# Optimization experiments

Hardware: AMD Instinct MI355X
Metric: run time of the kernel (lower is better)

## Reference

```python
import jax, jax.numpy as jnp
import numpy as np

# Pangu-Weather EarthSpecificBlock, layer-1 config
WZ, WH, WW = 2, 6, 12          # window size (z, lat, lon)
Z, H, W = 8, 91, 180           # token grid after patch embedding
C = 192                        # token dim
HEADS = 6
B = 1
PAD_TOP, PAD_BOT = 2, 3        # lat 91 -> 96 (CustomPad3d, centered)
ZP, HP, WP = 8, 96, 180        # padded grid
NWB = (ZP // WZ) * (HP // WH)  # 64 bias windows (z*lat)
N = WZ * WH * WW               # 144 tokens per window


def earth_position_index():
    zi = np.arange(WZ); zj = -np.arange(WZ) * WZ
    hi = np.arange(WH); hj = -np.arange(WH) * WH
    w = np.arange(WW)
    c1 = np.stack(np.meshgrid(zi, hi, w, indexing='ij')).reshape(3, -1)
    c2 = np.stack(np.meshgrid(zj, hj, w, indexing='ij')).reshape(3, -1)
    coords = (c1[:, :, None] - c2[:, None, :]).transpose(1, 2, 0).astype(np.int64)
    coords[:, :, 2] += WW - 1
    coords[:, :, 1] *= 2 * WW - 1
    coords[:, :, 0] *= (2 * WW - 1) * WH * WH
    return coords.sum(-1)  # (N, N) int indices into bias table

POS_IDX = jnp.asarray(earth_position_index())


def layer_norm(x, w, b, eps=1e-5):
    mu = x.mean(-1, keepdims=True)
    var = ((x - mu) ** 2).mean(-1, keepdims=True)
    return (x - mu) * jax.lax.rsqrt(var + eps) * w + b


def setup_inputs() -> dict:
    key = jax.random.key(0)
    ks = jax.random.split(key, 8)
    f = lambda k, s: jax.random.normal(k, s, jnp.float32) * 0.02
    return {
        "x": jax.random.normal(ks[0], (B, Z * H * W, C), jnp.float32),
        "qkv_w": f(ks[1], (3 * C, C)),
        "qkv_b": jnp.zeros((3 * C,), jnp.float32),
        "proj_w": f(ks[2], (C, C)),
        "proj_b": jnp.zeros((C,), jnp.float32),
        "bias_table": f(ks[3], ((2 * WW - 1) * WH * WH * WZ * WZ, NWB, HEADS)),
        "norm1_w": jnp.ones((C,), jnp.float32),
        "norm1_b": jnp.zeros((C,), jnp.float32),
        "norm2_w": jnp.ones((C,), jnp.float32),
        "norm2_b": jnp.zeros((C,), jnp.float32),
        "mlp_w1": f(ks[4], (4 * C, C)),
        "mlp_b1": jnp.zeros((4 * C,), jnp.float32),
        "mlp_w2": f(ks[5], (C, 4 * C)),
        "mlp_b2": jnp.zeros((C,), jnp.float32),
        "roll": 0,
    }


def reference(x, qkv_w, qkv_b, proj_w, proj_b, bias_table,
              norm1_w, norm1_b, norm2_w, norm2_b,
              mlp_w1, mlp_b1, mlp_w2, mlp_b2, roll):
    shortcut = x  # (B, L, C)
    hd = C // HEADS
    scale = hd ** -0.5
    xs = x.reshape(B, Z, H, W, C)
    xs = jnp.pad(xs, ((0, 0), (0, 0), (PAD_TOP, PAD_BOT), (0, 0), (0, 0)))
    # window partition: (B, ZP, HP, WP, C) -> (nb, N, C), windows ordered (z, lat, lon)
    xw = xs.reshape(B, ZP // WZ, WZ, HP // WH, WH, WP // WW, WW, C)
    xw = xw.transpose(0, 1, 3, 5, 2, 4, 6, 7).reshape(-1, N, C)
    nb = xw.shape[0]  # B * 64 * 15 = 960
    qkv = (xw @ qkv_w.T + qkv_b).reshape(nb, N, 3, HEADS, hd).transpose(2, 0, 3, 1, 4)
    q, k, v = qkv[0] * scale, qkv[1], qkv[2]  # each (nb, HEADS, N, hd)
    att = jnp.einsum('bhnd,bhmd->bhnm', q, k)  # (nb, HEADS, N, N)
    # earth-specific bias gathered via position index
    bias = bias_table[POS_IDX]                 # (N, N, NWB, HEADS)
    bias = bias.transpose(2, 3, 0, 1)          # (NWB, HEADS, N, N)
    # nb = B * NWB * n_lon_windows, NWB is the leading window factor
    att = att.reshape(B, NWB, -1, HEADS, N, N) + bias[None, :, None]
    att = jax.nn.softmax(att, axis=-1).reshape(nb, HEADS, N, N)
    out = jnp.einsum('bhnm,bhmd->bnhd', att, v).reshape(nb, N, C)
    out = out @ proj_w.T + proj_b
    # window reverse + crop padding
    out = out.reshape(B, ZP // WZ, HP // WH, WP // WW, WZ, WH, WW, C)
    out = out.transpose(0, 1, 4, 2, 5, 3, 6, 7).reshape(B, ZP, HP, WP, C)
    out = out[:, :, PAD_TOP:HP - PAD_BOT, :, :].reshape(B, -1, C)
    # post-norm residual (Pangu): x = shortcut + norm1(attn); x = x + norm2(mlp(x))
    x1 = shortcut + layer_norm(out, norm1_w, norm1_b)
    h1 = jax.nn.gelu(x1 @ mlp_w1.T + mlp_b1, approximate=False)
    mlp_out = h1 @ mlp_w2.T + mlp_b2
    return x1 + layer_norm(mlp_out, norm2_w, norm2_b)
```

## Files before the change

kernel.cpp:

```cpp
#include <hip/hip_runtime.h>
#include <hip/hip_bf16.h>

typedef __hip_bfloat16 bf16;
#define DEVI __device__ __forceinline__

typedef __bf16 bf16x8 __attribute__((ext_vector_type(8)));
typedef __bf16 bf16x4 __attribute__((ext_vector_type(4)));
typedef float  f32x4  __attribute__((ext_vector_type(4)));

DEVI float bf2f(bf16 v) { return __bfloat162float(v); }
DEVI bf16 f2bf(float v) { return __float2bfloat16(v); }

DEVI unsigned short bfbits(float x) {
    bf16 h = __float2bfloat16(x);
    return *reinterpret_cast<unsigned short*>(&h);
}
DEVI unsigned int pack2(float x, float y) {
    return (unsigned int)bfbits(x) | ((unsigned int)bfbits(y) << 16);
}
DEVI float2 unpack2(unsigned int u) {
    float2 r;
    r.x = __uint_as_float(u << 16);
    r.y = __uint_as_float(u & 0xffff0000u);
    return r;
}
DEVI bf16x8 pack8(float4 lo, float4 hi) {
    union { unsigned int u[4]; bf16x8 v; } z;
    z.u[0] = pack2(lo.x, lo.y); z.u[1] = pack2(lo.z, lo.w);
    z.u[2] = pack2(hi.x, hi.y); z.u[3] = pack2(hi.z, hi.w);
    return z.v;
}
DEVI bf16x8 ld8h(const bf16* p) {
    bf16x4 lo = *(const bf16x4*)p;
    bf16x4 hi = *(const bf16x4*)(p + 4);
    return __builtin_shufflevector(lo, hi, 0, 1, 2, 3, 4, 5, 6, 7);
}

__global__ __launch_bounds__(256) void prep_attn_w(
    const float* __restrict__ qkv_w, const float* __restrict__ qkv_b,
    bf16* __restrict__ qkv_wb, float* __restrict__ qkv_bb)
{
    const float scale = 0.17677669529663687f;
    int idx = blockIdx.x * 256 + threadIdx.x;
    if (idx < 110592) {
        int c = idx % 192, d = idx / 192;
        int h = d / 96, q2 = d - h * 96, seg = q2 >> 5, rr = q2 & 31;
        float v = qkv_w[(size_t)(seg * 192 + h * 32 + rr) * 192 + c];
        if (seg == 0) v *= scale;
        qkv_wb[idx] = f2bf(v);
    }
    if (idx < 576) {
        int h = idx / 96, q2 = idx - h * 96, seg = q2 >> 5, rr = q2 & 31;
        float b = qkv_b[seg * 192 + h * 32 + rr];
        if (seg == 0) b *= scale;
        qkv_bb[idx] = b;
    }
}

__global__ __launch_bounds__(256) void prep_bias(
    const float* __restrict__ bias_table, bf16* __restrict__ biasT)
{
    int idx = blockIdx.x * 256 + threadIdx.x;
    if (idx >= 7962624) return;
    int m = idx % 144;
    int n = (idx / 144) % 144;
    int r2 = idx / 20736;
    int h = r2 % 6, wb = r2 / 6;
    int tzn = n / 72, thn = (n / 12) % 6, twn = n % 12;
    int tzm = m / 72, thm = (m / 12) % 6, twm = m % 12;
    int bidx = (tzn + 2 * tzm) * 828 + (thn + 6 * thm) * 23 + (twn - twm + 11);
    biasT[idx] = f2bf(bias_table[(size_t)(bidx * 64 + wb) * 6 + h]);
}

__global__ __launch_bounds__(256, 2) void attn_mfma_kernel(
    const float* __restrict__ x, const bf16* __restrict__ qkv_wb,
    const float* __restrict__ qkv_bb, const bf16* __restrict__ biasT,
    bf16* __restrict__ attn_out)
{
    __shared__ alignas(16) char sm[79872];
    bf16* Qs  = (bf16*)sm;
    bf16* Ks  = (bf16*)(sm + 10368);
    bf16* VTs = (bf16*)(sm + 20736);
    bf16* Ps  = (bf16*)(sm + 31488);

    const int tid  = threadIdx.x;
    const int wave = tid >> 6;
    const int lane = tid & 63;
    const int quad = lane >> 4;
    const int l15  = lane & 15;
    const int wi   = blockIdx.x;
    const int head = blockIdx.y;
    const int ww_  = wi % 15;
    const int hw   = (wi / 15) % 16;
    const int zw   = wi / 240;
    const int wb   = zw * 16 + hw;

    for (int i = tid; i < 32 * 24; i += 256) {
        int d = i / 24, c = i - d * 24;
        VTs[d * 168 + 144 + c] = f2bf(0.f);
    }

    bf16x8 af[3][6];
#pragma unroll
    for (int i = 0; i < 3; ++i) {
        int mt = wave + 4 * i;
        if (mt < 9) {
            int t  = mt * 16 + l15;
            int tz = t / 72, rr = t - tz * 72;
            int th = rr / 12, tw = rr - th * 12;
            int lat = hw * 6 + th - 2;
            bool valid = (lat >= 0 && lat < 91);
            size_t base = ((size_t)((zw * 2 + tz) * 91 + (valid ? lat : 0)) * 180
                           + ww_ * 12 + tw) * 192;
#pragma unroll
            for (int ks = 0; ks < 6; ++ks) {
                float4 lo = make_float4(0.f, 0.f, 0.f, 0.f);
                float4 hi = make_float4(0.f, 0.f, 0.f, 0.f);
                if (valid) {
                    lo = *(const float4*)(x + base + ks * 32 + quad * 8);
                    hi = *(const float4*)(x + base + ks * 32 + quad * 8 + 4);
                }
                af[i][ks] = pack8(lo, hi);
            }
        }
    }

    for (int nt = 0; nt < 6; ++nt) {
        const bf16* wrow = qkv_wb + (size_t)(head * 96 + nt * 16 + l15) * 192;
        bf16x8 bw[6];
#pragma unroll
        for (int ks = 0; ks < 6; ++ks)
            bw[ks] = *(const bf16x8*)(wrow + ks * 32 + quad * 8);
        float bias = qkv_bb[head * 96 + nt * 16 + l15];

        f32x4 acc[3];
#pragma unroll
        for (int i = 0; i < 3; ++i) acc[i] = (f32x4){0.f, 0.f, 0.f, 0.f};
#pragma unroll
        for (int ks = 0; ks < 6; ++ks)
#pragma unroll
            for (int i = 0; i < 3; ++i) {
                int mt = wave + 4 * i;
                if (mt < 9)
                    acc[i] = __builtin_amdgcn_mfma_f32_16x16x32_bf16(
                        af[i][ks], bw[ks], acc[i], 0, 0, 0);
            }
#pragma unroll
        for (int i = 0; i < 3; ++i) {
            int mt = wave + 4 * i;
            if (mt < 9) {
#pragma unroll
                for (int r = 0; r < 4; ++r) {
                    float v = acc[i][r] + bias;
                    int tok = mt * 16 + quad * 4 + r;
                    if (nt < 2)      Qs[tok * 36 + nt * 16 + l15] = f2bf(v);
                    else if (nt < 4) Ks[tok * 36 + (nt - 2) * 16 + l15] = f2bf(v);
                    else             VTs[((nt - 4) * 16 + l15) * 168 + tok] = f2bf(v);
                }
            }
        }
    }
    __syncthreads();

    bf16x8 qa[3];
#pragma unroll
    for (int i = 0; i < 3; ++i) {
        int mt = wave + 4 * i;
        if (mt < 9) qa[i] = ld8h(Qs + (mt * 16 + l15) * 36 + quad * 8);
    }
    f32x4 sa[3][9];
    for (int nt = 0; nt < 9; ++nt) {
        bf16x8 kb = ld8h(Ks + (nt * 16 + l15) * 36 + quad * 8);
#pragma unroll
        for (int i = 0; i < 3; ++i) {
            int mt = wave + 4 * i;
            sa[i][nt] = (f32x4){0.f, 0.f, 0.f, 0.f};
            if (mt < 9)
                sa[i][nt] = __builtin_amdgcn_mfma_f32_16x16x32_bf16(
                    qa[i], kb, sa[i][nt], 0, 0, 0);
        }
    }
    const bf16* bt = biasT + (size_t)(wb * 6 + head) * 20736;
#pragma unroll
    for (int i = 0; i < 3; ++i) {
        int mt = wave + 4 * i;
        if (mt < 9) {
#pragma unroll
            for (int nt = 0; nt < 9; ++nt)
#pragma unroll
                for (int r = 0; r < 4; ++r) {
                    int row = mt * 16 + quad * 4 + r;
                    sa[i][nt][r] += bf2f(bt[row * 144 + nt * 16 + l15]);
                }
        }
    }

#pragma unroll
    for (int i = 0; i < 3; ++i) {
        int mt = wave + 4 * i;
        if (mt < 9) {
#pragma unroll
            for (int r = 0; r < 4; ++r) {
                float mx = -1e30f;
#pragma unroll
                for (int nt = 0; nt < 9; ++nt) mx = fmaxf(mx, sa[i][nt][r]);
#pragma unroll
                for (int msk = 1; msk < 16; msk <<= 1)
                    mx = fmaxf(mx, __shfl_xor(mx, msk, 64));
                float s = 0.f;
#pragma unroll
                for (int nt = 0; nt < 9; ++nt) {
                    float e = __expf(sa[i][nt][r] - mx);
                    sa[i][nt][r] = e;
                    s += e;
                }
#pragma unroll
                for (int msk = 1; msk < 16; msk <<= 1)
                    s += __shfl_xor(s, msk, 64);
                float inv = 1.f / s;
                int row = mt * 16 + quad * 4 + r;
#pragma unroll
                for (int nt = 0; nt < 9; ++nt)
                    Ps[row * 168 + nt * 16 + l15] = f2bf(sa[i][nt][r] * inv);
                Ps[row * 168 + 144 + l15] = f2bf(0.f);
            }
        }
    }

    f32x4 oa[3][2];
#pragma unroll
    for (int i = 0; i < 3; ++i)
#pragma unroll
        for (int n2 = 0; n2 < 2; ++n2) oa[i][n2] = (f32x4){0.f, 0.f, 0.f, 0.f};
#pragma unroll
    for (int ks = 0; ks < 5; ++ks) {
        bf16x8 vb[2];
#pragma unroll
        for (int n2 = 0; n2 < 2; ++n2)
            vb[n2] = *(const bf16x8*)(VTs + (n2 * 16 + l15) * 168 + ks * 32 + quad * 8);
#pragma unroll
        for (int i = 0; i < 3; ++i) {
            int mt = wave + 4 * i;
            if (mt < 9) {
                bf16x8 pa = *(const bf16x8*)(Ps + (mt * 16 + l15) * 168 + ks * 32 + quad * 8);
#pragma unroll
                for (int n2 = 0; n2 < 2; ++n2)
                    oa[i][n2] = __builtin_amdgcn_mfma_f32_16x16x32_bf16(
                        pa, vb[n2], oa[i][n2], 0, 0, 0);
            }
        }
    }

#pragma unroll
    for (int i = 0; i < 3; ++i) {
        int mt = wave + 4 * i;
        if (mt < 9) {
#pragma unroll
            for (int n2 = 0; n2 < 2; ++n2)
#pragma unroll
                for (int r = 0; r < 4; ++r) {
                    int tok = mt * 16 + quad * 4 + r;
                    attn_out[(size_t)(wi * 144 + tok) * 192 + (head << 5) + n2 * 16 + l15]
                        = f2bf(oa[i][n2][r]);
                }
        }
    }
}

__global__ __launch_bounds__(256, 2) void proj_mfma_kernel(
    const bf16* __restrict__ attn, const float* __restrict__ proj_w,
    const float* __restrict__ proj_b, const float* __restrict__ xin,
    const float* __restrict__ n1w, const float* __restrict__ n1b,
    bf16* __restrict__ x1out)
{
    __shared__ alignas(16) char sm[56320];
    bf16*  Xs     = (bf16*)sm;
    float* wsum   = (float*)(sm + 51200);
    float* wsq    = (float*)(sm + 53248);
    float* mean_s = (float*)(sm + 55296);
    float* rstd_s = (float*)(sm + 55808);

    const int tid  = threadIdx.x;
    const int wave = tid >> 6;
    const int lane = tid & 63;
    const int quad = lane >> 4;
    const int l15  = lane & 15;
    const long tok0 = (long)blockIdx.x * 128;
    const int colw = wave * 48;

    for (int i = tid; i < 128 * 24; i += 256) {
        int r = i / 24, c4 = i - r * 24;
        long l = tok0 + r;
        uint4 v = make_uint4(0u, 0u, 0u, 0u);
        if (l < 131040) {
            int li  = (int)l;
            int z   = li / 16380, rem = li - z * 16380;
            int lat = rem / 180, lon = rem - lat * 180;
            int latp = lat + 2;
            int zw = z >> 1, tz = z & 1;
            int hw = latp / 6, th = latp - hw * 6;
            int wwn = lon / 12, tw = lon - wwn * 12;
            int wi = (zw * 16 + hw) * 15 + wwn;
            int t  = (tz * 6 + th) * 12 + tw;
            v = *(const uint4*)(attn + (size_t)(wi * 144 + t) * 192 + c4 * 8);
        }
        *(uint4*)(Xs + r * 200 + c4 * 8) = v;
    }
    __syncthreads();

    f32x4 o[3][8];
#pragma unroll
    for (int nt = 0; nt < 3; ++nt)
#pragma unroll
        for (int mt = 0; mt < 8; ++mt)
            o[nt][mt] = (f32x4){0.f, 0.f, 0.f, 0.f};

#pragma unroll
    for (int ks = 0; ks < 6; ++ks) {
        bf16x8 wfr[3];
#pragma unroll
        for (int nt = 0; nt < 3; ++nt) {
            const float* wp = proj_w + (size_t)(colw + nt * 16 + l15) * 192
                            + ks * 32 + quad * 8;
            float4 lo = *(const float4*)wp;
            float4 hi = *(const float4*)(wp + 4);
            wfr[nt] = pack8(lo, hi);
        }
#pragma unroll
        for (int mt = 0; mt < 8; ++mt) {
            bf16x8 a = *(const bf16x8*)(Xs + (mt * 16 + l15) * 200 + ks * 32 + quad * 8);
#pragma unroll
            for (int nt = 0; nt < 3; ++nt)
                o[nt][mt] = __builtin_amdgcn_mfma_f32_16x16x32_bf16(
                    a, wfr[nt], o[nt][mt], 0, 0, 0);
        }
    }

    float pbv[3], gw[3], gb[3];
#pragma unroll
    for (int nt = 0; nt < 3; ++nt) {
        int c = colw + nt * 16 + l15;
        pbv[nt] = proj_b[c];
        gw[nt]  = n1w[c];
        gb[nt]  = n1b[c];
    }
#pragma unroll
    for (int nt = 0; nt < 3; ++nt)
#pragma unroll
        for (int mt = 0; mt < 8; ++mt)
#pragma unroll
            for (int r = 0; r < 4; ++r)
                o[nt][mt][r] += pbv[nt];

#pragma unroll
    for (int mt = 0; mt < 8; ++mt) {
#pragma unroll
        for (int r = 0; r < 4; ++r) {
            float p = o[0][mt][r] + o[1][mt][r] + o[2][mt][r];
            float q = o[0][mt][r] * o[0][mt][r] + o[1][mt][r] * o[1][mt][r]
                    + o[2][mt][r] * o[2][mt][r];
#pragma unroll
            for (int m_ = 1; m_ < 16; m_ <<= 1) {
                p += __shfl_xor(p, m_, 64);
                q += __shfl_xor(q, m_, 64);
            }
            if (l15 == 0) {
                int row = mt * 16 + quad * 4 + r;
                wsum[row * 4 + wave] = p;
                wsq [row * 4 + wave] = q;
            }
        }
    }
    __syncthreads();
    if (tid < 128) {
        float s  = wsum[tid * 4] + wsum[tid * 4 + 1] + wsum[tid * 4 + 2] + wsum[tid * 4 + 3];
        float ss = wsq [tid * 4] + wsq [tid * 4 + 1] + wsq [tid * 4 + 2] + wsq [tid * 4 + 3];
        float m = s * (1.f / 192.f);
        float var = ss * (1.f / 192.f) - m * m;
        mean_s[tid] = m;
        rstd_s[tid] = rsqrtf(fmaxf(var, 0.f) + 1e-5f);
    }
    __syncthreads();

#pragma unroll
    for (int mt = 0; mt < 8; ++mt) {
#pragma unroll
        for (int r = 0; r < 4; ++r) {
            int row = mt * 16 + quad * 4 + r;
            long tok = tok0 + row;
            if (tok < 131040) {
                float m = mean_s[row], rsd = rstd_s[row];
#pragma unroll
                for (int nt = 0; nt < 3; ++nt) {
                    int c = colw + nt * 16 + l15;
                    float val = (o[nt][mt][r] - m) * rsd * gw[nt] + gb[nt]
                              + xin[(size_t)tok * 192 + c];
                    x1out[(size_t)tok * 192 + c] = f2bf(val);
                }
            }
        }
    }
}

__global__ __launch_bounds__(256) void prep_weights(
    const float* __restrict__ w1, const float* __restrict__ w2,
    unsigned int* __restrict__ w1b, unsigned int* __restrict__ w2b)
{
    int i = blockIdx.x * 256 + threadIdx.x;
    if (i < 73728) {
        w1b[i] = pack2(w1[2 * i], w1[2 * i + 1]);
    } else {
        int j = i - 73728;
        w2b[j] = pack2(w2[2 * j], w2[2 * j + 1]);
    }
}

__global__ __launch_bounds__(256, 2) void mlp_mfma_kernel(
    const bf16* __restrict__ x1, const bf16* __restrict__ w1b,
    const float* __restrict__ b1, const bf16* __restrict__ w2b,
    const float* __restrict__ b2, const float* __restrict__ n2w,
    const float* __restrict__ n2b, float* __restrict__ out)
{
    __shared__ alignas(16) char sm[53760];
    bf16*  Xs     = (bf16*)sm;
    bf16*  Hs     = (bf16*)(sm + 25600);
    float* wsum   = (float*)(sm + 51200);
    float* wsq    = (float*)(sm + 52224);
    float* mean_s = (float*)(sm + 53248);
    float* rstd_s = (float*)(sm + 53504);

    const int tid  = threadIdx.x;
    const int wave = tid >> 6;
    const int lane = tid & 63;
    const int quad = lane >> 4;
    const int l15  = lane & 15;
    const long tok0 = (long)blockIdx.x * 64;
    const int colw = wave * 48;

    for (int i = tid; i < 64 * 24; i += 256) {
        int r = i / 24, c8 = i - r * 24;
        uint4 v = make_uint4(0u, 0u, 0u, 0u);
        if (tok0 + r < 131040)
            v = *(const uint4*)(x1 + (tok0 + r) * 192 + (size_t)c8 * 8);
        *(uint4*)(Xs + r * 200 + c8 * 8) = v;
    }
    __syncthreads();

    bf16x8 af[4][6];
#pragma unroll
    for (int mt = 0; mt < 4; ++mt)
#pragma unroll
        for (int ks = 0; ks < 6; ++ks)
            af[mt][ks] = *(const bf16x8*)(Xs + (mt * 16 + l15) * 200 + ks * 32 + quad * 8);

    f32x4 o[3][4];
#pragma unroll
    for (int nt = 0; nt < 3; ++nt)
#pragma unroll
        for (int mt = 0; mt < 4; ++mt)
            o[nt][mt] = (f32x4){0.f, 0.f, 0.f, 0.f};

    for (int nc = 0; nc < 4; ++nc) {
        f32x4 g[3][4];
#pragma unroll
        for (int nt = 0; nt < 3; ++nt)
#pragma unroll
            for (int mt = 0; mt < 4; ++mt)
                g[nt][mt] = (f32x4){0.f, 0.f, 0.f, 0.f};
        const int h0 = nc * 192 + colw;
#pragma unroll
        for (int ks = 0; ks < 6; ++ks) {
            bf16x8 bfr[3];
#pragma unroll
            for (int nt = 0; nt < 3; ++nt)
                bfr[nt] = *(const bf16x8*)(w1b + (size_t)(h0 + nt * 16 + l15) * 192 + ks * 32 + quad * 8);
#pragma unroll
            for (int nt = 0; nt < 3; ++nt)
#pragma unroll
                for (int mt = 0; mt < 4; ++mt)
                    g[nt][mt] = __builtin_amdgcn_mfma_f32_16x16x32_bf16(
                        af[mt][ks], bfr[nt], g[nt][mt], 0, 0, 0);
        }
        __syncthreads();

#pragma unroll
        for (int nt = 0; nt < 3; ++nt) {
            float bb = b1[h0 + nt * 16 + l15];
            int hcol = colw + nt * 16 + l15;
#pragma unroll
            for (int mt = 0; mt < 4; ++mt) {
#pragma unroll
                for (int r = 0; r < 4; ++r) {
                    float v = g[nt][mt][r] + bb;
                    float u = v * (0.7978845608028654f + 0.035677408136300125f * v * v);
                    float e = __expf(2.f * u);
                    float t = 1.f - 2.f / (e + 1.f);
                    float gl = 0.5f * v * (1.f + t);
                    Hs[(mt * 16 + quad * 4 + r) * 200 + hcol] = f2bf(gl);
                }
            }
        }
        __syncthreads();

#pragma unroll
        for (int ks = 0; ks < 6; ++ks) {
            bf16x8 hf[4];
#pragma unroll
            for (int mt = 0; mt < 4; ++mt)
                hf[mt] = *(const bf16x8*)(Hs + (mt * 16 + l15) * 200 + ks * 32 + quad * 8);
            bf16x8 wf[3];
#pragma unroll
            for (int nt = 0; nt < 3; ++nt)
                wf[nt] = *(const bf16x8*)(w2b + (size_t)(colw + nt * 16 + l15) * 768 + nc * 192 + ks * 32 + quad * 8);
#pragma unroll
            for (int nt = 0; nt < 3; ++nt)
#pragma unroll
                for (int mt = 0; mt < 4; ++mt)
                    o[nt][mt] = __builtin_amdgcn_mfma_f32_16x16x32_bf16(
                        hf[mt], wf[nt], o[nt][mt], 0, 0, 0);
        }
    }

    float b2v[3], gw[3], gb[3];
#pragma unroll
    for (int nt = 0; nt < 3; ++nt) {
        int c = colw + nt * 16 + l15;
        b2v[nt] = b2[c];
        gw[nt] = n2w[c];
        gb[nt] = n2b[c];
    }
#pragma unroll
    for (int nt = 0; nt < 3; ++nt)
#pragma unroll
        for (int mt = 0; mt < 4; ++mt)
#pragma unroll
            for (int r = 0; r < 4; ++r)
                o[nt][mt][r] += b2v[nt];

#pragma unroll
    for (int mt = 0; mt < 4; ++mt) {
#pragma unroll
        for (int r = 0; r < 4; ++r) {
            float p = o[0][mt][r] + o[1][mt][r] + o[2][mt][r];
            float q = o[0][mt][r] * o[0][mt][r] + o[1][mt][r] * o[1][mt][r]
                    + o[2][mt][r] * o[2][mt][r];
#pragma unroll
            for (int m_ = 1; m_ < 16; m_ <<= 1) {
                p += __shfl_xor(p, m_, 64);
                q += __shfl_xor(q, m_, 64);
            }
            if (l15 == 0) {
                int row = mt * 16 + quad * 4 + r;
                wsum[row * 4 + wave] = p;
                wsq [row * 4 + wave] = q;
            }
        }
    }
    __syncthreads();
    if (tid < 64) {
        float s  = wsum[tid * 4] + wsum[tid * 4 + 1] + wsum[tid * 4 + 2] + wsum[tid * 4 + 3];
        float ss = wsq [tid * 4] + wsq [tid * 4 + 1] + wsq [tid * 4 + 2] + wsq [tid * 4 + 3];
        float m = s * (1.f / 192.f);
        float var = ss * (1.f / 192.f) - m * m;
        mean_s[tid] = m;
        rstd_s[tid] = rsqrtf(fmaxf(var, 0.f) + 1e-5f);
    }
    __syncthreads();

#pragma unroll
    for (int mt = 0; mt < 4; ++mt) {
#pragma unroll
        for (int r = 0; r < 4; ++r) {
            int row = mt * 16 + quad * 4 + r;
            long tok = tok0 + row;
            if (tok < 131040) {
                float m = mean_s[row], rsd = rstd_s[row];
#pragma unroll
                for (int nt = 0; nt < 3; ++nt) {
                    int c = colw + nt * 16 + l15;
                    float val = (o[nt][mt][r] - m) * rsd * gw[nt] + gb[nt]
                              + bf2f(Xs[row * 200 + c]);
                    out[tok * 192 + c] = val;
                }
            }
        }
    }
}

extern "C" void kernel_launch(void* const* d_in, const int* in_sizes, int n_in,
                              void* d_out, int out_size, void* d_ws, size_t ws_size,
                              hipStream_t stream) {
    (void)in_sizes; (void)n_in; (void)out_size; (void)ws_size;
    const float* x          = (const float*)d_in[0];
    const float* qkv_w      = (const float*)d_in[1];
    const float* qkv_b      = (const float*)d_in[2];
    const float* proj_w     = (const float*)d_in[3];
    const float* proj_b     = (const float*)d_in[4];
    const float* bias_table = (const float*)d_in[5];
    const float* n1w        = (const float*)d_in[6];
    const float* n1b        = (const float*)d_in[7];
    const float* n2w        = (const float*)d_in[8];
    const float* n2b        = (const float*)d_in[9];
    const float* w1         = (const float*)d_in[10];
    const float* b1         = (const float*)d_in[11];
    const float* w2         = (const float*)d_in[12];
    const float* b2         = (const float*)d_in[13];
    float* out = (float*)d_out;

    bf16*  attn_ws = (bf16*)d_ws;
    bf16*  x1_ws   = (bf16*)((char*)d_ws + 53084160);
    bf16*  w1b     = (bf16*)d_ws;
    bf16*  w2b     = (bf16*)((char*)d_ws + 294912);
    bf16*  qkv_wb  = (bf16*)((char*)d_ws + 53084160);
    float* qkv_bb  = (float*)((char*)d_ws + 53305344);
    bf16*  biasT   = (bf16*)((char*)d_ws + 53307648);

    prep_attn_w<<<432, 256, 0, stream>>>(qkv_w, qkv_b, qkv_wb, qkv_bb);
    prep_bias<<<31104, 256, 0, stream>>>(bias_table, biasT);
    attn_mfma_kernel<<<dim3(960, 6), 256, 0, stream>>>(x, qkv_wb, qkv_bb, biasT, attn_ws);
    proj_mfma_kernel<<<1024, 256, 0, stream>>>(attn_ws, proj_w, proj_b, x, n1w, n1b, x1_ws);
    prep_weights<<<576, 256, 0, stream>>>(w1, w2, (unsigned int*)w1b, (unsigned int*)w2b);
    mlp_mfma_kernel<<<2048, 256, 0, stream>>>(x1_ws, w1b, b1, w2b, b2, n2w, n2b, out);
}
```

Before: 755.0 us.

## Keep softmax probabilities in registers via transposed QK^T and lane shuffles

The attention kernel now computes S^T = K·Q^T, so each lane holds a query column and the softmax reduction needs only two cross-quad shuffles. The normalized probabilities are packed to bf16 and rearranged with lane shuffles into MFMA A-operand fragments instead of being written to and reread from a shared-memory P buffer. This cuts LDS use from about 78KB to 31KB and raises launch bounds to 3 blocks per CU. The grid is also flattened and remapped with an XCD-aware swizzle so the six heads of a window land on the same XCD. The tradeoff is extra register pressure and shuffle work in the PV stage.

```diff
diff --git a/kernel.cpp b/kernel.cpp
--- a/kernel.cpp
+++ b/kernel.cpp
@@ -17,12 +17,6 @@
 }
 DEVI unsigned int pack2(float x, float y) {
     return (unsigned int)bfbits(x) | ((unsigned int)bfbits(y) << 16);
-}
-DEVI float2 unpack2(unsigned int u) {
-    float2 r;
-    r.x = __uint_as_float(u << 16);
-    r.y = __uint_as_float(u & 0xffff0000u);
-    return r;
 }
 DEVI bf16x8 pack8(float4 lo, float4 hi) {
     union { unsigned int u[4]; bf16x8 v; } z;
@@ -62,42 +56,44 @@
 {
     int idx = blockIdx.x * 256 + threadIdx.x;
     if (idx >= 7962624) return;
-    int m = idx % 144;
-    int n = (idx / 144) % 144;
+    int t = idx % 144;
+    int k = (idx / 144) % 144;
     int r2 = idx / 20736;
     int h = r2 % 6, wb = r2 / 6;
-    int tzn = n / 72, thn = (n / 12) % 6, twn = n % 12;
-    int tzm = m / 72, thm = (m / 12) % 6, twm = m % 12;
-    int bidx = (tzn + 2 * tzm) * 828 + (thn + 6 * thm) * 23 + (twn - twm + 11);
+    int tzq = t / 72, thq = (t / 12) % 6, twq = t % 12;
+    int tzk = k / 72, thk = (k / 12) % 6, twk = k % 12;
+    int bidx = (tzq + 2 * tzk) * 828 + (thq + 6 * thk) * 23 + (twq - twk + 11);
     biasT[idx] = f2bf(bias_table[(size_t)(bidx * 64 + wb) * 6 + h]);
 }
 
-__global__ __launch_bounds__(256, 2) void attn_mfma_kernel(
+__global__ __launch_bounds__(256, 3) void attn_mfma_kernel(
     const float* __restrict__ x, const bf16* __restrict__ qkv_wb,
     const float* __restrict__ qkv_bb, const bf16* __restrict__ biasT,
     bf16* __restrict__ attn_out)
 {
-    __shared__ alignas(16) char sm[79872];
+    __shared__ alignas(16) char sm[30976];
     bf16* Qs  = (bf16*)sm;
     bf16* Ks  = (bf16*)(sm + 10368);
     bf16* VTs = (bf16*)(sm + 20736);
-    bf16* Ps  = (bf16*)(sm + 31488);
 
     const int tid  = threadIdx.x;
     const int wave = tid >> 6;
     const int lane = tid & 63;
     const int quad = lane >> 4;
     const int l15  = lane & 15;
-    const int wi   = blockIdx.x;
-    const int head = blockIdx.y;
+
+    const int bid     = blockIdx.x;
+    const int logical = (bid & 7) * 720 + (bid >> 3);
+    const int wi      = logical / 6;
+    const int head    = logical % 6;
     const int ww_  = wi % 15;
     const int hw   = (wi / 15) % 16;
     const int zw   = wi / 240;
     const int wb   = zw * 16 + hw;
 
-    for (int i = tid; i < 32 * 24; i += 256) {
-        int d = i / 24, c = i - d * 24;
-        VTs[d * 168 + 144 + c] = f2bf(0.f);
+    for (int i = tid; i < 512; i += 256) {
+        int d = i >> 4, c = i & 15;
+        VTs[d * 160 + 144 + c] = f2bf(0.f);
     }
 
     bf16x8 af[3][6];
@@ -155,111 +151,130 @@
                     int tok = mt * 16 + quad * 4 + r;
                     if (nt < 2)      Qs[tok * 36 + nt * 16 + l15] = f2bf(v);
                     else if (nt < 4) Ks[tok * 36 + (nt - 2) * 16 + l15] = f2bf(v);
-                    else             VTs[((nt - 4) * 16 + l15) * 168 + tok] = f2bf(v);
+                    else             VTs[((nt - 4) * 16 + l15) * 160 + tok] = f2bf(v);
                 }
             }
         }
     }
     __syncthreads();
 
-    bf16x8 qa[3];
+    bf16x8 qb[3];
 #pragma unroll
     for (int i = 0; i < 3; ++i) {
-        int mt = wave + 4 * i;
-        if (mt < 9) qa[i] = ld8h(Qs + (mt * 16 + l15) * 36 + quad * 8);
-    }
-    f32x4 sa[3][9];
-    for (int nt = 0; nt < 9; ++nt) {
-        bf16x8 kb = ld8h(Ks + (nt * 16 + l15) * 36 + quad * 8);
+        int nti = wave + 4 * i;
+        if (nti < 9) qb[i] = ld8h(Qs + (nti * 16 + l15) * 36 + quad * 8);
+    }
+    f32x4 st[3][9];
+#pragma unroll
+    for (int mt = 0; mt < 9; ++mt) {
+        bf16x8 ka = ld8h(Ks + (mt * 16 + l15) * 36 + quad * 8);
 #pragma unroll
         for (int i = 0; i < 3; ++i) {
-            int mt = wave + 4 * i;
-            sa[i][nt] = (f32x4){0.f, 0.f, 0.f, 0.f};
-            if (mt < 9)
-                sa[i][nt] = __builtin_amdgcn_mfma_f32_16x16x32_bf16(
-                    qa[i], kb, sa[i][nt], 0, 0, 0);
-        }
-    }
+            int nti = wave + 4 * i;
+            st[i][mt] = (f32x4){0.f, 0.f, 0.f, 0.f};
+            if (nti < 9)
+                st[i][mt] = __builtin_amdgcn_mfma_f32_16x16x32_bf16(
+                    ka, qb[i], st[i][mt], 0, 0, 0);
+        }
+    }
+
     const bf16* bt = biasT + (size_t)(wb * 6 + head) * 20736;
 #pragma unroll
     for (int i = 0; i < 3; ++i) {
-        int mt = wave + 4 * i;
-        if (mt < 9) {
-#pragma unroll
-            for (int nt = 0; nt < 9; ++nt)
+        int nti = wave + 4 * i;
+        if (nti < 9) {
+#pragma unroll
+            for (int mt = 0; mt < 9; ++mt)
+#pragma unroll
+                for (int r = 0; r < 4; ++r)
+                    st[i][mt][r] += bf2f(bt[(mt * 16 + quad * 4 + r) * 144
+                                            + nti * 16 + l15]);
+        }
+    }
+
+#pragma unroll
+    for (int i = 0; i < 3; ++i) {
+        int nti = wave + 4 * i;
+        if (nti < 9) {
+            float mx = -1e30f;
+#pragma unroll
+            for (int mt = 0; mt < 9; ++mt)
+#pragma unroll
+                for (int r = 0; r < 4; ++r) mx = fmaxf(mx, st[i][mt][r]);
+            mx = fmaxf(mx, __shfl_xor(mx, 16, 64));
+            mx = fmaxf(mx, __shfl_xor(mx, 32, 64));
+            float s = 0.f;
+#pragma unroll
+            for (int mt = 0; mt < 9; ++mt)
 #pragma unroll
                 for (int r = 0; r < 4; ++r) {
-                    int row = mt * 16 + quad * 4 + r;
-                    sa[i][nt][r] += bf2f(bt[row * 144 + nt * 16 + l15]);
-                }
-        }
-    }
+                    float e = __expf(st[i][mt][r] - mx);
+                    st[i][mt][r] = e;
+                    s += e;
+                }
+            s += __shfl_xor(s, 16, 64);
+            s += __shfl_xor(s, 32, 64);
+            float inv = 1.f / s;
+#pragma unroll
+            for (int mt = 0; mt < 9; ++mt)
+#pragma unroll
+                for (int r = 0; r < 4; ++r) st[i][mt][r] *= inv;
+        }
+    }
+
+    f32x4 oa[3][2];
+#pragma unroll
+    for (int i = 0; i < 3; ++i)
+#pragma unroll
+        for (int n2 = 0; n2 < 2; ++n2) oa[i][n2] = (f32x4){0.f, 0.f, 0.f, 0.f};
 
 #pragma unroll
     for (int i = 0; i < 3; ++i) {
-        int mt = wave + 4 * i;
-        if (mt < 9) {
-#pragma unroll
-            for (int r = 0; r < 4; ++r) {
-                float mx = -1e30f;
-#pragma unroll
-                for (int nt = 0; nt < 9; ++nt) mx = fmaxf(mx, sa[i][nt][r]);
-#pragma unroll
-                for (int msk = 1; msk < 16; msk <<= 1)
-                    mx = fmaxf(mx, __shfl_xor(mx, msk, 64));
-                float s = 0.f;
-#pragma unroll
-                for (int nt = 0; nt < 9; ++nt) {
-                    float e = __expf(sa[i][nt][r] - mx);
-                    sa[i][nt][r] = e;
-                    s += e;
-                }
-#pragma unroll
-                for (int msk = 1; msk < 16; msk <<= 1)
-                    s += __shfl_xor(s, msk, 64);
-                float inv = 1.f / s;
-                int row = mt * 16 + quad * 4 + r;
-#pragma unroll
-                for (int nt = 0; nt < 9; ++nt)
-                    Ps[row * 168 + nt * 16 + l15] = f2bf(sa[i][nt][r] * inv);
-                Ps[row * 168 + 144 + l15] = f2bf(0.f);
-            }
-        }
-    }
-
-    f32x4 oa[3][2];
-#pragma unroll
-    for (int i = 0; i < 3; ++i)
-#pragma unroll
-        for (int n2 = 0; n2 < 2; ++n2) oa[i][n2] = (f32x4){0.f, 0.f, 0.f, 0.f};
-#pragma unroll
-    for (int ks = 0; ks < 5; ++ks) {
-        bf16x8 vb[2];
-#pragma unroll
-        for (int n2 = 0; n2 < 2; ++n2)
-            vb[n2] = *(const bf16x8*)(VTs + (n2 * 16 + l15) * 168 + ks * 32 + quad * 8);
-#pragma unroll
-        for (int i = 0; i < 3; ++i) {
-            int mt = wave + 4 * i;
-            if (mt < 9) {
-                bf16x8 pa = *(const bf16x8*)(Ps + (mt * 16 + l15) * 168 + ks * 32 + quad * 8);
-#pragma unroll
-                for (int n2 = 0; n2 < 2; ++n2)
+        int nti = wave + 4 * i;
+        if (nti < 9) {
+#pragma unroll
+            for (int ks = 0; ks < 5; ++ks) {
+                unsigned A0 = pack2(st[i][2 * ks][0], st[i][2 * ks][1]);
+                unsigned A1 = pack2(st[i][2 * ks][2], st[i][2 * ks][3]);
+                unsigned B0 = 0u, B1 = 0u;
+                if (ks < 4) {
+                    B0 = pack2(st[i][2 * ks + 1][0], st[i][2 * ks + 1][1]);
+                    B1 = pack2(st[i][2 * ks + 1][2], st[i][2 * ks + 1][3]);
+                }
+                bool lo2 = quad < 2;
+                unsigned Z0 = lo2 ? A0 : B0, Z1 = lo2 ? A1 : B1;
+                unsigned Y0 = lo2 ? B0 : A0, Y1 = lo2 ? B1 : A1;
+                unsigned s16_0 = __shfl_xor((int)Z0, 16, 64);
+                unsigned s16_1 = __shfl_xor((int)Z1, 16, 64);
+                unsigned s32_0 = __shfl_xor((int)Y0, 32, 64);
+                unsigned s32_1 = __shfl_xor((int)Y1, 32, 64);
+                unsigned s48_0 = __shfl_xor((int)Y0, 48, 64);
+                unsigned s48_1 = __shfl_xor((int)Y1, 48, 64);
+                union { unsigned u[4]; bf16x8 v; } fr;
+                fr.u[0] = (quad == 0) ? Z0 : (quad == 1) ? s48_0 : (quad == 2) ? s32_0 : s16_0;
+                fr.u[1] = (quad == 0) ? Z1 : (quad == 1) ? s48_1 : (quad == 2) ? s32_1 : s16_1;
+                fr.u[2] = (quad == 0) ? s16_0 : (quad == 1) ? s32_0 : (quad == 2) ? s48_0 : Z0;
+                fr.u[3] = (quad == 0) ? s16_1 : (quad == 1) ? s32_1 : (quad == 2) ? s48_1 : Z1;
+#pragma unroll
+                for (int n2 = 0; n2 < 2; ++n2) {
+                    bf16x8 vb = *(const bf16x8*)(VTs + (n2 * 16 + l15) * 160
+                                                 + ks * 32 + quad * 8);
                     oa[i][n2] = __builtin_amdgcn_mfma_f32_16x16x32_bf16(
-                        pa, vb[n2], oa[i][n2], 0, 0, 0);
+                        fr.v, vb, oa[i][n2], 0, 0, 0);
+                }
             }
         }
     }
 
 #pragma unroll
     for (int i = 0; i < 3; ++i) {
-        int mt = wave + 4 * i;
-        if (mt < 9) {
+        int nti = wave + 4 * i;
+        if (nti < 9) {
 #pragma unroll
             for (int n2 = 0; n2 < 2; ++n2)
 #pragma unroll
                 for (int r = 0; r < 4; ++r) {
-                    int tok = mt * 16 + quad * 4 + r;
+                    int tok = nti * 16 + quad * 4 + r;
                     attn_out[(size_t)(wi * 144 + tok) * 192 + (head << 5) + n2 * 16 + l15]
                         = f2bf(oa[i][n2][r]);
                 }
@@ -617,7 +632,7 @@
 
     prep_attn_w<<<432, 256, 0, stream>>>(qkv_w, qkv_b, qkv_wb, qkv_bb);
     prep_bias<<<31104, 256, 0, stream>>>(bias_table, biasT);
-    attn_mfma_kernel<<<dim3(960, 6), 256, 0, stream>>>(x, qkv_wb, qkv_bb, biasT, attn_ws);
+    attn_mfma_kernel<<<5760, 256, 0, stream>>>(x, qkv_wb, qkv_bb, biasT, attn_ws);
     proj_mfma_kernel<<<1024, 256, 0, stream>>>(attn_ws, proj_w, proj_b, x, n1w, n1b, x1_ws);
     prep_weights<<<576, 256, 0, stream>>>(w1, w2, (unsigned int*)w1b, (unsigned int*)w2b);
     mlp_mfma_kernel<<<2048, 256, 0, stream>>>(x1_ws, w1b, b1, w2b, b2, n2w, n2b, out);
```

New measurement: 783.6 us. 1.04x slower.
